# Kernel optimization log

Measured on AMD Instinct MI355X. Metric: run time of the kernel, lower is better.

Reference implementation:

```python
import jax, jax.numpy as jnp
import numpy as np

N = 100000
E = 1600000
D = 128
BN_EPS = 1e-5


def setup_inputs() -> dict:
    key = jax.random.key(0)
    ks = jax.random.split(key, 12)
    s = 1.0 / np.sqrt(D)
    x = jax.random.normal(ks[0], (N, D), dtype=jnp.float32)
    edge_index = jax.random.randint(ks[1], (2, E), 0, N, dtype=jnp.int64)
    # Linear weights stored as [in, out] (i.e. torch W.T)
    w1a = jax.random.uniform(ks[2], (D, D), jnp.float32, -s, s)
    b1a = jax.random.uniform(ks[3], (D,), jnp.float32, -s, s)
    w1b = jax.random.uniform(ks[4], (D, D), jnp.float32, -s, s)
    b1b = jax.random.uniform(ks[5], (D,), jnp.float32, -s, s)
    gamma2 = jnp.ones((D,), jnp.float32)
    beta2 = jnp.zeros((D,), jnp.float32)
    w2a = jax.random.uniform(ks[6], (D, D), jnp.float32, -s, s)
    b2a = jax.random.uniform(ks[7], (D,), jnp.float32, -s, s)
    w2b = jax.random.uniform(ks[8], (D, D), jnp.float32, -s, s)
    b2b = jax.random.uniform(ks[9], (D,), jnp.float32, -s, s)
    return dict(x=x, edge_index=edge_index, w1a=w1a, b1a=b1a, w1b=w1b, b1b=b1b,
                gamma2=gamma2, beta2=beta2, w2a=w2a, b2a=b2a, w2b=w2b, b2b=b2b)


def _gin_conv(h, src, dst, wa, ba, wb, bb):
    # GINConv (eps=0): nn(sum_{j in N(i)} h_j + h_i), then 2-layer MLP
    agg = jax.ops.segment_sum(h[src], dst, num_segments=h.shape[0])
    z = agg + h
    z = jax.nn.relu(z @ wa + ba)
    return z @ wb + bb


def reference(x, edge_index, w1a, b1a, w1b, b1b, gamma2, beta2, w2a, b2a, w2b, b2b):
    src, dst = edge_index[0], edge_index[1]
    h = _gin_conv(x, src, dst, w1a, b1a, w1b, b1b)
    h = jax.nn.relu(h)
    # BatchNorm1d in training mode: batch mean / biased variance
    mean = jnp.mean(h, axis=0)
    var = jnp.mean((h - mean) ** 2, axis=0)
    h = (h - mean) * jax.lax.rsqrt(var + BN_EPS) * gamma2 + beta2
    return _gin_conv(h, src, dst, w2a, b2a, w2b, b2b)
```

## Files before the change

kernel.cpp:

```cpp
#include <hip/hip_runtime.h>

#define NNODES 100000
#define NEDGES 1600000
#define DIM 128
#define BN_EPS 1e-5f
#define NBUCK 1024
#define NB_USED ((NNODES + 127) / 128)

typedef unsigned int uint;
typedef unsigned short ushort_t;
using bhalf8  = __attribute__((ext_vector_type(8))) short;
using u16x8   = __attribute__((ext_vector_type(8))) unsigned short;
using f32x4_t = __attribute__((ext_vector_type(4))) float;

__device__ __forceinline__ float bf2f(uint u16) {
    return __uint_as_float(u16 << 16);
}
__device__ __forceinline__ uint pack2_bf16rn(float a, float b) {
    uint ua = __float_as_uint(a); ua += 0x7FFFu + ((ua >> 16) & 1u);
    uint ub = __float_as_uint(b); ub += 0x7FFFu + ((ub >> 16) & 1u);
    return __builtin_amdgcn_perm(ub, ua, 0x07060302u);
}

__device__ __forceinline__ int edge_src(const int* ei, int fl, int e) {
    return fl ? ei[2 * e] : ei[e];
}
__device__ __forceinline__ int edge_dst(const int* ei, int fl, int e) {
    return fl ? ei[2 * (NEDGES + e)] : ei[NEDGES + e];
}

__global__ __launch_bounds__(256) void k_prep(const float* __restrict__ X,
                                              const int* __restrict__ ei,
                                              const float* __restrict__ w0,
                                              const float* __restrict__ w1,
                                              const float* __restrict__ w2,
                                              const float* __restrict__ w3,
                                              float* __restrict__ stats,
                                              int* __restrict__ flag,
                                              int* __restrict__ bcnt,
                                              ushort_t* __restrict__ wbuf,
                                              ushort_t* __restrict__ Xb) {
    int bid = blockIdx.x;
    int t = threadIdx.x;
    if (bid < 4) {
        const float* w = (bid == 0) ? w0 : (bid == 1) ? w1 : (bid == 2) ? w2 : w3;
        ushort_t* oh = wbuf + (size_t)bid * 16384;
        for (int i = t; i < 16384; i += 256) {
            int k = i >> 7, n = i & 127;
            uint u = __float_as_uint(w[i]);
            u += 0x7FFFu + ((u >> 16) & 1u);
            oh[n * 128 + k] = (ushort_t)(u >> 16);
        }
    } else if (bid == 4) {
        stats[t] = 0.0f;
        ((int4*)bcnt)[t] = make_int4(0, 0, 0, 0);
        if (t == 0) {
            int orr = 0;
            for (int i = 1; i < 128; i += 2) orr |= ei[i];
            *flag = (orr == 0) ? 1 : 0;
        }
    } else {
        size_t i = ((size_t)(bid - 5) * 256 + t) * 8;
        float4 a = *(const float4*)(X + i);
        float4 b = *(const float4*)(X + i + 4);
        union { uint4 q; u16x8 v; } o;
        o.q.x = pack2_bf16rn(a.x, a.y);
        o.q.y = pack2_bf16rn(a.z, a.w);
        o.q.z = pack2_bf16rn(b.x, b.y);
        o.q.w = pack2_bf16rn(b.z, b.w);
        *(u16x8*)(Xb + i) = o.v;
    }
}

__global__ __launch_bounds__(256) void k_bcount(const int* __restrict__ ei,
                                                const int* __restrict__ flag,
                                                int* __restrict__ bcnt) {
    __shared__ int h[NBUCK];
    int t = threadIdx.x;
    for (int i = t; i < NBUCK; i += 256) h[i] = 0;
    __syncthreads();
    int fl = *flag;
    int per = (NEDGES + gridDim.x - 1) / gridDim.x;
    int e0 = blockIdx.x * per;
    int e1 = min(e0 + per, NEDGES);
    for (int e = e0 + t; e < e1; e += 256)
        atomicAdd(&h[edge_dst(ei, fl, e) >> 7], 1);
    __syncthreads();
    for (int i = t; i < NBUCK; i += 256)
        if (h[i]) atomicAdd(&bcnt[i], h[i]);
}

__global__ __launch_bounds__(256) void k_bscan(const int* __restrict__ bcnt,
                                               int* __restrict__ bstart,
                                               int* __restrict__ bcur) {
    __shared__ int wtot[4];
    int t = threadIdx.x, lane = t & 63, w = t >> 6;
    int4 v = ((const int4*)bcnt)[t];
    int s = v.x + v.y + v.z + v.w;
    int sc = s;
#pragma unroll
    for (int d = 1; d < 64; d <<= 1) {
        int n = __shfl_up(sc, d, 64);
        if (lane >= d) sc += n;
    }
    if (lane == 63) wtot[w] = sc;
    __syncthreads();
    int woff = 0;
    for (int i = 0; i < w; ++i) woff += wtot[i];
    int excl = woff + sc - s;
    int o0 = excl, o1 = o0 + v.x, o2 = o1 + v.y, o3 = o2 + v.z;
    bstart[t * 4]     = o0;  bcur[t * 4]     = o0;
    bstart[t * 4 + 1] = o1;  bcur[t * 4 + 1] = o1;
    bstart[t * 4 + 2] = o2;  bcur[t * 4 + 2] = o2;
    bstart[t * 4 + 3] = o3;  bcur[t * 4 + 3] = o3;
    if (t == 255) bstart[NBUCK] = o3 + v.w;
}

__global__ __launch_bounds__(256) void k_bpair(const int* __restrict__ ei,
                                               const int* __restrict__ flag,
                                               int* __restrict__ bcur,
                                               int* __restrict__ pairs) {
    __shared__ int h[NBUCK];
    __shared__ int base[NBUCK];
    int t = threadIdx.x;
    for (int i = t; i < NBUCK; i += 256) h[i] = 0;
    __syncthreads();
    int fl = *flag;
    int per = (NEDGES + gridDim.x - 1) / gridDim.x;
    int e0 = blockIdx.x * per;
    int e1 = min(e0 + per, NEDGES);
    for (int e = e0 + t; e < e1; e += 256)
        atomicAdd(&h[edge_dst(ei, fl, e) >> 7], 1);
    __syncthreads();
    for (int i = t; i < NBUCK; i += 256) {
        int c = h[i];
        base[i] = c ? atomicAdd(&bcur[i], c) : 0;
    }
    __syncthreads();
    for (int i = t; i < NBUCK; i += 256) h[i] = 0;
    __syncthreads();
    for (int e = e0 + t; e < e1; e += 256) {
        int s = edge_src(ei, fl, e);
        int d = edge_dst(ei, fl, e);
        int b = d >> 7;
        int pos = atomicAdd(&h[b], 1);
        pairs[base[b] + pos] = (s << 7) | (d & 127);
    }
}

__global__ __launch_bounds__(256) void k_bsort(const int* __restrict__ pairs,
                                               const int* __restrict__ bstart,
                                               int* __restrict__ C,
                                               int* __restrict__ ssrc) {
    __shared__ int cnt[2048];
    __shared__ int off[2048];
    __shared__ int wtot[4];
    int b = blockIdx.x;
    int t = threadIdx.x, lane = t & 63, w = t >> 6;
    int s = bstart[b], e = bstart[b + 1];
    for (int i = t; i < 2048; i += 256) cnt[i] = 0;
    __syncthreads();
    for (int i = s + t; i < e; i += 256) {
        int p = pairs[i];
        atomicAdd(&cnt[(p & 127) * 16 + (p >> 20)], 1);
    }
    __syncthreads();
    int base = t * 8, loc[8], sum = 0;
#pragma unroll
    for (int j = 0; j < 8; ++j) { loc[j] = cnt[base + j]; sum += loc[j]; }
    int sc = sum;
#pragma unroll
    for (int d = 1; d < 64; d <<= 1) {
        int n = __shfl_up(sc, d, 64);
        if (lane >= d) sc += n;
    }
    if (lane == 63) wtot[w] = sc;
    __syncthreads();
    int woff = 0;
    for (int i = 0; i < w; ++i) woff += wtot[i];
    int run = woff + sc - sum;
#pragma unroll
    for (int j = 0; j < 8; ++j) { off[base + j] = run; run += loc[j]; }
    __syncthreads();
    if (t < 128) {
        int row = b * 128 + t;
        if (row < NNODES) C[row] = s + off[t * 16 + 15] + cnt[t * 16 + 15];
    }
    __syncthreads();
    for (int i = s + t; i < e; i += 256) {
        int p = pairs[i];
        int k = (p & 127) * 16 + (p >> 20);
        int pos = atomicAdd(&off[k], 1);
        ssrc[s + pos] = p >> 7;
    }
}

__device__ __forceinline__ void split8(const float4& f0, const float4& f1,
                                       bhalf8& h, bhalf8& l) {
    uint u[8] = { __float_as_uint(f0.x), __float_as_uint(f0.y),
                  __float_as_uint(f0.z), __float_as_uint(f0.w),
                  __float_as_uint(f1.x), __float_as_uint(f1.y),
                  __float_as_uint(f1.z), __float_as_uint(f1.w) };
    float fv[8] = { f0.x, f0.y, f0.z, f0.w, f1.x, f1.y, f1.z, f1.w };
    uint lu[8];
#pragma unroll
    for (int i = 0; i < 8; ++i) {
        float hf = __uint_as_float(u[i] & 0xffff0000u);
        lu[i] = __float_as_uint(fv[i] - hf);
    }
    union { uint4 q; bhalf8 s; } H, L;
    H.q.x = __builtin_amdgcn_perm(u[1], u[0], 0x07060302u);
    H.q.y = __builtin_amdgcn_perm(u[3], u[2], 0x07060302u);
    H.q.z = __builtin_amdgcn_perm(u[5], u[4], 0x07060302u);
    H.q.w = __builtin_amdgcn_perm(u[7], u[6], 0x07060302u);
    L.q.x = __builtin_amdgcn_perm(lu[1], lu[0], 0x07060302u);
    L.q.y = __builtin_amdgcn_perm(lu[3], lu[2], 0x07060302u);
    L.q.z = __builtin_amdgcn_perm(lu[5], lu[4], 0x07060302u);
    L.q.w = __builtin_amdgcn_perm(lu[7], lu[6], 0x07060302u);
    h = H.s; l = L.s;
}

template <bool BN, bool SELF_F32>
__global__ __launch_bounds__(256) void k_agg(const ushort_t* __restrict__ Xb,
                                             const float* __restrict__ Xf,
                                             float* __restrict__ Z,
                                             const int* __restrict__ ends,
                                             const int* __restrict__ ssrc,
                                             const float* __restrict__ stats,
                                             const float* __restrict__ gamma,
                                             const float* __restrict__ beta) {
    __shared__ float scs[128], shs[128];
    int t = threadIdx.x;
    if (BN) {
        if (t < 128) {
            float s  = stats[t];
            float sq = stats[128 + t];
            float mean = s / (float)NNODES;
            float var  = sq / (float)NNODES - mean * mean;
            float sc = gamma[t] * rsqrtf(var + BN_EPS);
            scs[t] = sc;
            shs[t] = beta[t] - mean * sc;
        }
        __syncthreads();
    }
    int g = t >> 4;
    int l = t & 15;
    int row = blockIdx.x * 16 + g;
    int c8 = l * 8;
    int start = (row == 0) ? 0 : ends[row - 1];
    int end = ends[row];

    float acc[8];
    if (SELF_F32) {
        float4 a0 = *(const float4*)(Xf + (size_t)row * DIM + c8);
        float4 a1 = *(const float4*)(Xf + (size_t)row * DIM + c8 + 4);
        acc[0] = a0.x; acc[1] = a0.y; acc[2] = a0.z; acc[3] = a0.w;
        acc[4] = a1.x; acc[5] = a1.y; acc[6] = a1.z; acc[7] = a1.w;
    } else {
        union { u16x8 v; uint u[4]; } sv;
        sv.v = *(const u16x8*)(Xb + (size_t)row * DIM + c8);
#pragma unroll
        for (int i = 0; i < 4; ++i) {
            acc[2 * i]     = bf2f(sv.u[i] & 0xffffu);
            acc[2 * i + 1] = __uint_as_float(sv.u[i] & 0xffff0000u);
        }
    }

    int e = start;
    for (; e + 7 < end; e += 8) {
        union { u16x8 v; uint u[4]; } nv[8];
#pragma unroll
        for (int i = 0; i < 8; ++i) {
            int s0 = ssrc[e + i];
            nv[i].v = *(const u16x8*)(Xb + (size_t)s0 * DIM + c8);
        }
#pragma unroll
        for (int i = 0; i < 8; ++i) {
#pragma unroll
            for (int j = 0; j < 4; ++j) {
                acc[2 * j]     += bf2f(nv[i].u[j] & 0xffffu);
                acc[2 * j + 1] += __uint_as_float(nv[i].u[j] & 0xffff0000u);
            }
        }
    }
    for (; e < end; ++e) {
        int s0 = ssrc[e];
        union { u16x8 v; uint u[4]; } nv;
        nv.v = *(const u16x8*)(Xb + (size_t)s0 * DIM + c8);
#pragma unroll
        for (int j = 0; j < 4; ++j) {
            acc[2 * j]     += bf2f(nv.u[j] & 0xffffu);
            acc[2 * j + 1] += __uint_as_float(nv.u[j] & 0xffff0000u);
        }
    }

    if (BN) {
        float4 sc0 = *(const float4*)(scs + c8);
        float4 sc1 = *(const float4*)(scs + c8 + 4);
        float4 sh0 = *(const float4*)(shs + c8);
        float4 sh1 = *(const float4*)(shs + c8 + 4);
        float cnt = (float)(end - start + 1);
        acc[0] = fmaf(acc[0], sc0.x, cnt * sh0.x);
        acc[1] = fmaf(acc[1], sc0.y, cnt * sh0.y);
        acc[2] = fmaf(acc[2], sc0.z, cnt * sh0.z);
        acc[3] = fmaf(acc[3], sc0.w, cnt * sh0.w);
        acc[4] = fmaf(acc[4], sc1.x, cnt * sh1.x);
        acc[5] = fmaf(acc[5], sc1.y, cnt * sh1.y);
        acc[6] = fmaf(acc[6], sc1.z, cnt * sh1.z);
        acc[7] = fmaf(acc[7], sc1.w, cnt * sh1.w);
    }
    float* zp = Z + (size_t)row * DIM + c8;
    *(float4*)zp       = make_float4(acc[0], acc[1], acc[2], acc[3]);
    *(float4*)(zp + 4) = make_float4(acc[4], acc[5], acc[6], acc[7]);
}

template <bool CONV1>
__global__ __launch_bounds__(256, 2) void k_mlp(const float* __restrict__ Z,
                                                const ushort_t* __restrict__ WAh,
                                                const ushort_t* __restrict__ WBh,
                                                const float* __restrict__ Ba,
                                                const float* __restrict__ Bb,
                                                float* __restrict__ OutF,
                                                ushort_t* __restrict__ OutB,
                                                float* __restrict__ stats) {
    __shared__ ushort_t wsl[16384];
    __shared__ float hbuf[64 * 128];
    __shared__ float lsum[128], lsq[128];
    char* hb = (char*)hbuf;

    int t = threadIdx.x;
    int w = t >> 6, l = t & 63;
    int lr = l & 15;
    int lg = l >> 4;
    int slane = (lr & 7) << 4;
    if (CONV1 && t < 128) { lsum[t] = 0.f; lsq[t] = 0.f; }

    int rowBase = blockIdx.x * 64 + w * 16;
    bool active = rowBase < NNODES;

#pragma unroll
    for (int i = 0; i < 8; ++i) {
        int c = i * 256 + t;
        uint4 v = ((const uint4*)WAh)[c];
        ((uint4*)wsl)[c ^ ((c >> 4) & 7)] = v;
    }
    int zrow = active ? (rowBase + lr) : 0;
    const float* zp = Z + (size_t)zrow * 128 + lg * 8;
    float4 zf[8];
#pragma unroll
    for (int ks = 0; ks < 4; ++ks) {
        zf[2 * ks]     = *(const float4*)(zp + ks * 32);
        zf[2 * ks + 1] = *(const float4*)(zp + ks * 32 + 4);
    }
    f32x4_t acc[8];
#pragma unroll
    for (int nt = 0; nt < 8; ++nt) {
        float b = Ba[nt * 16 + lr];
        acc[nt][0] = b; acc[nt][1] = b; acc[nt][2] = b; acc[nt][3] = b;
    }
    bhalf8 zh[4], zl[4];
#pragma unroll
    for (int ks = 0; ks < 4; ++ks) split8(zf[2 * ks], zf[2 * ks + 1], zh[ks], zl[ks]);
    __syncthreads();

#pragma unroll
    for (int ks = 0; ks < 4; ++ks) {
#pragma unroll
        for (int nt = 0; nt < 8; ++nt) {
            int waddr = ((nt * 16 + lr) << 8) + ((((ks << 6) + (lg << 4))) ^ slane);
            bhalf8 wh = *(const bhalf8*)((const char*)wsl + waddr);
            acc[nt] = __builtin_amdgcn_mfma_f32_16x16x32_bf16(zh[ks], wh, acc[nt], 0, 0, 0);
            acc[nt] = __builtin_amdgcn_mfma_f32_16x16x32_bf16(zl[ks], wh, acc[nt], 0, 0, 0);
        }
    }
#pragma unroll
    for (int nt = 0; nt < 8; ++nt) {
#pragma unroll
        for (int j = 0; j < 4; ++j) {
            int rl = w * 16 + lg * 4 + j;
            int boff = (rl * 512 + (nt * 16 + lr) * 4) ^ ((rl & 7) << 4);
            *(float*)(hb + boff) = fmaxf(acc[nt][j], 0.f);
        }
    }
    __syncthreads();

#pragma unroll
    for (int i = 0; i < 8; ++i) {
        int c = i * 256 + t;
        uint4 v = ((const uint4*)WBh)[c];
        ((uint4*)wsl)[c ^ ((c >> 4) & 7)] = v;
    }
    {
        int rl = w * 16 + lr;
        int swz = (rl & 7) << 4;
        int rbase = rl * 512 + lg * 32;
        float4 mf[8];
#pragma unroll
        for (int ks = 0; ks < 4; ++ks) {
            mf[2 * ks]     = *(const float4*)(hb + ((rbase + ks * 128) ^ swz));
            mf[2 * ks + 1] = *(const float4*)(hb + ((rbase + ks * 128 + 16) ^ swz));
        }
#pragma unroll
        for (int ks = 0; ks < 4; ++ks) split8(mf[2 * ks], mf[2 * ks + 1], zh[ks], zl[ks]);
    }
#pragma unroll
    for (int nt = 0; nt < 8; ++nt) {
        float b = Bb[nt * 16 + lr];
        acc[nt][0] = b; acc[nt][1] = b; acc[nt][2] = b; acc[nt][3] = b;
    }
    __syncthreads();

#pragma unroll
    for (int ks = 0; ks < 4; ++ks) {
#pragma unroll
        for (int nt = 0; nt < 8; ++nt) {
            int waddr = ((nt * 16 + lr) << 8) + ((((ks << 6) + (lg << 4))) ^ slane);
            bhalf8 wh = *(const bhalf8*)((const char*)wsl + waddr);
            acc[nt] = __builtin_amdgcn_mfma_f32_16x16x32_bf16(zh[ks], wh, acc[nt], 0, 0, 0);
            acc[nt] = __builtin_amdgcn_mfma_f32_16x16x32_bf16(zl[ks], wh, acc[nt], 0, 0, 0);
        }
    }

    if (CONV1 && active) {
#pragma unroll
        for (int nt = 0; nt < 8; ++nt) {
            float s = 0.f, q = 0.f;
#pragma unroll
            for (int j = 0; j < 4; ++j) {
                float v = fmaxf(acc[nt][j], 0.f);
                acc[nt][j] = v;
                s += v; q += v * v;
            }
            s += __shfl_xor(s, 16); s += __shfl_xor(s, 32);
            q += __shfl_xor(q, 16); q += __shfl_xor(q, 32);
            if (l < 16) {
                atomicAdd(&lsum[nt * 16 + l], s);
                atomicAdd(&lsq[nt * 16 + l], q);
            }
        }
    }
    __syncthreads();
#pragma unroll
    for (int nt = 0; nt < 8; ++nt) {
#pragma unroll
        for (int j = 0; j < 4; ++j) {
            int rl = w * 16 + lg * 4 + j;
            int boff = (rl * 512 + (nt * 16 + lr) * 4) ^ ((rl & 7) << 4);
            *(float*)(hb + boff) = acc[nt][j];
        }
    }
    if (CONV1) {
        __syncthreads();
        if (t < 128) {
            unsafeAtomicAdd(&stats[t], lsum[t]);
            unsafeAtomicAdd(&stats[128 + t], lsq[t]);
        }
    } else {
        __syncthreads();
    }
    {
        int r2 = t >> 2;
        int row = blockIdx.x * 64 + r2;
        if (row < NNODES) {
            int sw2 = (r2 & 7) << 4;
            int ch0 = (t & 3) * 8;
            if (CONV1) {
#pragma unroll
                for (int c = 0; c < 8; c += 2) {
                    float4 v0 = *(const float4*)(hb + ((r2 * 512 + (ch0 + c) * 16) ^ sw2));
                    float4 v1 = *(const float4*)(hb + ((r2 * 512 + (ch0 + c + 1) * 16) ^ sw2));
                    union { uint4 q; u16x8 v; } o;
                    o.q.x = pack2_bf16rn(v0.x, v0.y);
                    o.q.y = pack2_bf16rn(v0.z, v0.w);
                    o.q.z = pack2_bf16rn(v1.x, v1.y);
                    o.q.w = pack2_bf16rn(v1.z, v1.w);
                    *(u16x8*)(OutB + (size_t)row * 128 + (ch0 + c) * 4) = o.v;
                }
            } else {
#pragma unroll
                for (int c = 0; c < 8; ++c) {
                    float4 v = *(const float4*)(hb + ((r2 * 512 + (ch0 + c) * 16) ^ sw2));
                    *(float4*)(OutF + (size_t)row * 128 + (ch0 + c) * 4) = v;
                }
            }
        }
    }
}

extern "C" void kernel_launch(void* const* d_in, const int* in_sizes, int n_in,
                              void* d_out, int out_size, void* d_ws, size_t ws_size,
                              hipStream_t stream) {
    const float* x     = (const float*)d_in[0];
    const int*   ei    = (const int*)d_in[1];
    const float* w1a   = (const float*)d_in[2];
    const float* b1a   = (const float*)d_in[3];
    const float* w1b   = (const float*)d_in[4];
    const float* b1b   = (const float*)d_in[5];
    const float* gamma = (const float*)d_in[6];
    const float* beta  = (const float*)d_in[7];
    const float* w2a   = (const float*)d_in[8];
    const float* b2a   = (const float*)d_in[9];
    const float* w2b   = (const float*)d_in[10];
    const float* b2b   = (const float*)d_in[11];
    float* out = (float*)d_out;

    char*     ws     = (char*)d_ws;
    float*    stats  = (float*)ws;
    int*      flag   = (int*)(ws + 1024);
    int*      bcnt   = (int*)(ws + 4096);
    int*      bstart = (int*)(ws + 8192);
    int*      bcur   = (int*)(ws + 16384);
    int*      C      = (int*)(ws + 404096);
    int*      ssrc   = (int*)(ws + 804096);
    ushort_t* wbuf   = (ushort_t*)(ws + 0x700000);
    float*    zbuf   = (float*)(ws + 0x800000);
    int*      pairs  = (int*)(ws + 0x800000);

    ushort_t* xb  = (ushort_t*)d_out;
    ushort_t* hrb = (ushort_t*)d_out + (size_t)NNODES * DIM;

    const int aggBlocks  = NNODES / 16;
    const int prepBlocks = 5 + NNODES * DIM / (256 * 8);
    const int mlpBlocks  = (NNODES + 63) / 64;

    k_prep<<<prepBlocks, 256, 0, stream>>>(x, ei, w1a, w1b, w2a, w2b,
                                           stats, flag, bcnt, wbuf, xb);
    k_bcount<<<256, 256, 0, stream>>>(ei, flag, bcnt);
    k_bscan<<<1, 256, 0, stream>>>(bcnt, bstart, bcur);
    k_bpair<<<256, 256, 0, stream>>>(ei, flag, bcur, pairs);
    k_bsort<<<NB_USED, 256, 0, stream>>>(pairs, bstart, C, ssrc);
    k_agg<false, true><<<aggBlocks, 256, 0, stream>>>(xb, x, zbuf, C, ssrc,
                                                      nullptr, nullptr, nullptr);
    k_mlp<true><<<mlpBlocks, 256, 0, stream>>>(
        zbuf, wbuf, wbuf + 16384, b1a, b1b, nullptr, hrb, stats);
    k_agg<true, false><<<aggBlocks, 256, 0, stream>>>(hrb, nullptr, zbuf, C, ssrc,
                                                      stats, gamma, beta);
    k_mlp<false><<<mlpBlocks, 256, 0, stream>>>(
        zbuf, wbuf + 32768, wbuf + 49152, b2a, b2b, out, nullptr, nullptr);
}
```

Baseline: 306.1 us.

## Store aggregates in bf16, drop hi/lo split MFMAs, fuse histogram into prep

Result: no change. 305.4 us (-0.3%).

```diff
diff --git a/kernel.cpp b/kernel.cpp
--- a/kernel.cpp
+++ b/kernel.cpp
@@ -6,6 +6,7 @@
 #define BN_EPS 1e-5f
 #define NBUCK 1024
 #define NB_USED ((NNODES + 127) / 128)
+#define HISTB 64
 
 typedef unsigned int uint;
 typedef unsigned short ushort_t;
@@ -15,6 +16,11 @@
 
 __device__ __forceinline__ float bf2f(uint u16) {
     return __uint_as_float(u16 << 16);
+}
+__device__ __forceinline__ ushort_t f2bf(float f) {
+    uint u = __float_as_uint(f);
+    u += 0x7FFFu + ((u >> 16) & 1u);
+    return (ushort_t)(u >> 16);
 }
 __device__ __forceinline__ uint pack2_bf16rn(float a, float b) {
     uint ua = __float_as_uint(a); ua += 0x7FFFu + ((ua >> 16) & 1u);
@@ -37,9 +43,11 @@
                                               const float* __restrict__ w3,
                                               float* __restrict__ stats,
                                               int* __restrict__ flag,
-                                              int* __restrict__ bcnt,
+                                              int* __restrict__ parts,
                                               ushort_t* __restrict__ wbuf,
                                               ushort_t* __restrict__ Xb) {
+    __shared__ int h[NBUCK];
+    const int XB = NNODES * DIM / (256 * 8);
     int bid = blockIdx.x;
     int t = threadIdx.x;
     if (bid < 4) {
@@ -47,19 +55,16 @@
         ushort_t* oh = wbuf + (size_t)bid * 16384;
         for (int i = t; i < 16384; i += 256) {
             int k = i >> 7, n = i & 127;
-            uint u = __float_as_uint(w[i]);
-            u += 0x7FFFu + ((u >> 16) & 1u);
-            oh[n * 128 + k] = (ushort_t)(u >> 16);
+            oh[n * 128 + k] = f2bf(w[i]);
         }
     } else if (bid == 4) {
         stats[t] = 0.0f;
-        ((int4*)bcnt)[t] = make_int4(0, 0, 0, 0);
         if (t == 0) {
             int orr = 0;
             for (int i = 1; i < 128; i += 2) orr |= ei[i];
             *flag = (orr == 0) ? 1 : 0;
         }
-    } else {
+    } else if (bid < 5 + XB) {
         size_t i = ((size_t)(bid - 5) * 256 + t) * 8;
         float4 a = *(const float4*)(X + i);
         float4 b = *(const float4*)(X + i + 4);
@@ -69,33 +74,32 @@
         o.q.z = pack2_bf16rn(b.x, b.y);
         o.q.w = pack2_bf16rn(b.z, b.w);
         *(u16x8*)(Xb + i) = o.v;
-    }
-}
-
-__global__ __launch_bounds__(256) void k_bcount(const int* __restrict__ ei,
-                                                const int* __restrict__ flag,
-                                                int* __restrict__ bcnt) {
-    __shared__ int h[NBUCK];
-    int t = threadIdx.x;
-    for (int i = t; i < NBUCK; i += 256) h[i] = 0;
-    __syncthreads();
-    int fl = *flag;
-    int per = (NEDGES + gridDim.x - 1) / gridDim.x;
-    int e0 = blockIdx.x * per;
-    int e1 = min(e0 + per, NEDGES);
-    for (int e = e0 + t; e < e1; e += 256)
-        atomicAdd(&h[edge_dst(ei, fl, e) >> 7], 1);
-    __syncthreads();
-    for (int i = t; i < NBUCK; i += 256)
-        if (h[i]) atomicAdd(&bcnt[i], h[i]);
-}
-
-__global__ __launch_bounds__(256) void k_bscan(const int* __restrict__ bcnt,
+    } else {
+        int hb = bid - 5 - XB;
+        for (int i = t; i < NBUCK; i += 256) h[i] = 0;
+        __syncthreads();
+        int orr = 0;
+#pragma unroll
+        for (int i = 1; i < 64; i += 2) orr |= ei[i];
+        int fl = (orr == 0) ? 1 : 0;
+        int e0 = hb * (NEDGES / HISTB), e1 = e0 + NEDGES / HISTB;
+        for (int e = e0 + t; e < e1; e += 256)
+            atomicAdd(&h[edge_dst(ei, fl, e) >> 7], 1);
+        __syncthreads();
+        for (int i = t; i < NBUCK; i += 256) parts[hb * NBUCK + i] = h[i];
+    }
+}
+
+__global__ __launch_bounds__(256) void k_bscan(const int* __restrict__ parts,
                                                int* __restrict__ bstart,
                                                int* __restrict__ bcur) {
     __shared__ int wtot[4];
     int t = threadIdx.x, lane = t & 63, w = t >> 6;
-    int4 v = ((const int4*)bcnt)[t];
+    int4 v = make_int4(0, 0, 0, 0);
+    for (int b = 0; b < HISTB; ++b) {
+        int4 p = ((const int4*)(parts + b * NBUCK))[t];
+        v.x += p.x; v.y += p.y; v.z += p.z; v.w += p.w;
+    }
     int s = v.x + v.y + v.z + v.w;
     int sc = s;
 #pragma unroll
@@ -195,35 +199,10 @@
     }
 }
 
-__device__ __forceinline__ void split8(const float4& f0, const float4& f1,
-                                       bhalf8& h, bhalf8& l) {
-    uint u[8] = { __float_as_uint(f0.x), __float_as_uint(f0.y),
-                  __float_as_uint(f0.z), __float_as_uint(f0.w),
-                  __float_as_uint(f1.x), __float_as_uint(f1.y),
-                  __float_as_uint(f1.z), __float_as_uint(f1.w) };
-    float fv[8] = { f0.x, f0.y, f0.z, f0.w, f1.x, f1.y, f1.z, f1.w };
-    uint lu[8];
-#pragma unroll
-    for (int i = 0; i < 8; ++i) {
-        float hf = __uint_as_float(u[i] & 0xffff0000u);
-        lu[i] = __float_as_uint(fv[i] - hf);
-    }
-    union { uint4 q; bhalf8 s; } H, L;
-    H.q.x = __builtin_amdgcn_perm(u[1], u[0], 0x07060302u);
-    H.q.y = __builtin_amdgcn_perm(u[3], u[2], 0x07060302u);
-    H.q.z = __builtin_amdgcn_perm(u[5], u[4], 0x07060302u);
-    H.q.w = __builtin_amdgcn_perm(u[7], u[6], 0x07060302u);
-    L.q.x = __builtin_amdgcn_perm(lu[1], lu[0], 0x07060302u);
-    L.q.y = __builtin_amdgcn_perm(lu[3], lu[2], 0x07060302u);
-    L.q.z = __builtin_amdgcn_perm(lu[5], lu[4], 0x07060302u);
-    L.q.w = __builtin_amdgcn_perm(lu[7], lu[6], 0x07060302u);
-    h = H.s; l = L.s;
-}
-
 template <bool BN, bool SELF_F32>
 __global__ __launch_bounds__(256) void k_agg(const ushort_t* __restrict__ Xb,
                                              const float* __restrict__ Xf,
-                                             float* __restrict__ Z,
+                                             ushort_t* __restrict__ Zb,
                                              const int* __restrict__ ends,
                                              const int* __restrict__ ssrc,
                                              const float* __restrict__ stats,
@@ -309,24 +288,27 @@
         acc[6] = fmaf(acc[6], sc1.z, cnt * sh1.z);
         acc[7] = fmaf(acc[7], sc1.w, cnt * sh1.w);
     }
-    float* zp = Z + (size_t)row * DIM + c8;
-    *(float4*)zp       = make_float4(acc[0], acc[1], acc[2], acc[3]);
-    *(float4*)(zp + 4) = make_float4(acc[4], acc[5], acc[6], acc[7]);
+    union { uint4 q; u16x8 v; } o;
+    o.q.x = pack2_bf16rn(acc[0], acc[1]);
+    o.q.y = pack2_bf16rn(acc[2], acc[3]);
+    o.q.z = pack2_bf16rn(acc[4], acc[5]);
+    o.q.w = pack2_bf16rn(acc[6], acc[7]);
+    *(u16x8*)(Zb + (size_t)row * DIM + c8) = o.v;
 }
 
 template <bool CONV1>
-__global__ __launch_bounds__(256, 2) void k_mlp(const float* __restrict__ Z,
-                                                const ushort_t* __restrict__ WAh,
-                                                const ushort_t* __restrict__ WBh,
-                                                const float* __restrict__ Ba,
-                                                const float* __restrict__ Bb,
-                                                float* __restrict__ OutF,
-                                                ushort_t* __restrict__ OutB,
-                                                float* __restrict__ stats) {
+__global__ __launch_bounds__(256, CONV1 ? 3 : 2)
+void k_mlp(const ushort_t* __restrict__ Z,
+           const ushort_t* __restrict__ WAh,
+           const ushort_t* __restrict__ WBh,
+           const float* __restrict__ Ba,
+           const float* __restrict__ Bb,
+           float* __restrict__ OutF,
+           ushort_t* __restrict__ OutB,
+           float* __restrict__ stats) {
     __shared__ ushort_t wsl[16384];
-    __shared__ float hbuf[64 * 128];
+    __shared__ char hstage[CONV1 ? 16384 : 32768];
     __shared__ float lsum[128], lsq[128];
-    char* hb = (char*)hbuf;
 
     int t = threadIdx.x;
     int w = t >> 6, l = t & 63;
@@ -345,22 +327,16 @@
         ((uint4*)wsl)[c ^ ((c >> 4) & 7)] = v;
     }
     int zrow = active ? (rowBase + lr) : 0;
-    const float* zp = Z + (size_t)zrow * 128 + lg * 8;
-    float4 zf[8];
-#pragma unroll
-    for (int ks = 0; ks < 4; ++ks) {
-        zf[2 * ks]     = *(const float4*)(zp + ks * 32);
-        zf[2 * ks + 1] = *(const float4*)(zp + ks * 32 + 4);
-    }
+    const ushort_t* zp = Z + (size_t)zrow * 128 + lg * 8;
+    bhalf8 za[4];
+#pragma unroll
+    for (int ks = 0; ks < 4; ++ks) za[ks] = *(const bhalf8*)(zp + ks * 32);
     f32x4_t acc[8];
 #pragma unroll
     for (int nt = 0; nt < 8; ++nt) {
         float b = Ba[nt * 16 + lr];
         acc[nt][0] = b; acc[nt][1] = b; acc[nt][2] = b; acc[nt][3] = b;
     }
-    bhalf8 zh[4], zl[4];
-#pragma unroll
-    for (int ks = 0; ks < 4; ++ks) split8(zf[2 * ks], zf[2 * ks + 1], zh[ks], zl[ks]);
     __syncthreads();
 
 #pragma unroll
@@ -369,8 +345,7 @@
         for (int nt = 0; nt < 8; ++nt) {
             int waddr = ((nt * 16 + lr) << 8) + ((((ks << 6) + (lg << 4))) ^ slane);
             bhalf8 wh = *(const bhalf8*)((const char*)wsl + waddr);
-            acc[nt] = __builtin_amdgcn_mfma_f32_16x16x32_bf16(zh[ks], wh, acc[nt], 0, 0, 0);
-            acc[nt] = __builtin_amdgcn_mfma_f32_16x16x32_bf16(zl[ks], wh, acc[nt], 0, 0, 0);
+            acc[nt] = __builtin_amdgcn_mfma_f32_16x16x32_bf16(za[ks], wh, acc[nt], 0, 0, 0);
         }
     }
 #pragma unroll
@@ -378,8 +353,8 @@
 #pragma unroll
         for (int j = 0; j < 4; ++j) {
             int rl = w * 16 + lg * 4 + j;
-            int boff = (rl * 512 + (nt * 16 + lr) * 4) ^ ((rl & 7) << 4);
-            *(float*)(hb + boff) = fmaxf(acc[nt][j], 0.f);
+            int boff = (rl * 256 + (nt * 16 + lr) * 2) ^ ((rl & 7) << 4);
+            *(ushort_t*)(hstage + boff) = f2bf(fmaxf(acc[nt][j], 0.f));
         }
     }
     __syncthreads();
@@ -393,15 +368,9 @@
     {
         int rl = w * 16 + lr;
         int swz = (rl & 7) << 4;
-        int rbase = rl * 512 + lg * 32;
-        float4 mf[8];
-#pragma unroll
-        for (int ks = 0; ks < 4; ++ks) {
-            mf[2 * ks]     = *(const float4*)(hb + ((rbase + ks * 128) ^ swz));
-            mf[2 * ks + 1] = *(const float4*)(hb + ((rbase + ks * 128 + 16) ^ swz));
-        }
-#pragma unroll
-        for (int ks = 0; ks < 4; ++ks) split8(mf[2 * ks], mf[2 * ks + 1], zh[ks], zl[ks]);
+#pragma unroll
+        for (int ks = 0; ks < 4; ++ks)
+            za[ks] = *(const bhalf8*)(hstage + ((rl * 256 + (ks * 64 + lg * 16)) ^ swz));
     }
 #pragma unroll
     for (int nt = 0; nt < 8; ++nt) {
@@ -416,8 +385,7 @@
         for (int nt = 0; nt < 8; ++nt) {
             int waddr = ((nt * 16 + lr) << 8) + ((((ks << 6) + (lg << 4))) ^ slane);
             bhalf8 wh = *(const bhalf8*)((const char*)wsl + waddr);
-            acc[nt] = __builtin_amdgcn_mfma_f32_16x16x32_bf16(zh[ks], wh, acc[nt], 0, 0, 0);
-            acc[nt] = __builtin_amdgcn_mfma_f32_16x16x32_bf16(zl[ks], wh, acc[nt], 0, 0, 0);
+            acc[nt] = __builtin_amdgcn_mfma_f32_16x16x32_bf16(za[ks], wh, acc[nt], 0, 0, 0);
         }
     }
 
@@ -440,48 +408,52 @@
         }
     }
     __syncthreads();
-#pragma unroll
-    for (int nt = 0; nt < 8; ++nt) {
-#pragma unroll
-        for (int j = 0; j < 4; ++j) {
-            int rl = w * 16 + lg * 4 + j;
-            int boff = (rl * 512 + (nt * 16 + lr) * 4) ^ ((rl & 7) << 4);
-            *(float*)(hb + boff) = acc[nt][j];
-        }
-    }
     if (CONV1) {
+#pragma unroll
+        for (int nt = 0; nt < 8; ++nt) {
+#pragma unroll
+            for (int j = 0; j < 4; ++j) {
+                int rl = w * 16 + lg * 4 + j;
+                int boff = (rl * 256 + (nt * 16 + lr) * 2) ^ ((rl & 7) << 4);
+                *(ushort_t*)(hstage + boff) = f2bf(acc[nt][j]);
+            }
+        }
         __syncthreads();
         if (t < 128) {
             unsafeAtomicAdd(&stats[t], lsum[t]);
             unsafeAtomicAdd(&stats[128 + t], lsq[t]);
         }
+        int r2 = t >> 2;
+        int row = blockIdx.x * 64 + r2;
+        if (row < NNODES) {
+            int sw2 = (r2 & 7) << 4;
+#pragma unroll
+            for (int u = 0; u < 4; ++u) {
+                int uu = (t & 3) * 4 + u;
+                uint4 v = *(const uint4*)(hstage + ((r2 * 256 + uu * 16) ^ sw2));
+                *(uint4*)(OutB + (size_t)row * 128 + uu * 8) = v;
+            }
+        }
     } else {
+#pragma unroll
+        for (int nt = 0; nt < 8; ++nt) {
+#pragma unroll
+            for (int j = 0; j < 4; ++j) {
+                int rl = w * 16 + lg * 4 + j;
+                int boff = (rl * 512 + (nt * 16 + lr) * 4) ^ ((rl & 7) << 4);
+                *(float*)(hstage + boff) = acc[nt][j];
+            }
+        }
         __syncthreads();
-    }
-    {
         int r2 = t >> 2;
         int row = blockIdx.x * 64 + r2;
         if (row < NNODES) {
             int sw2 = (r2 & 7) << 4;
             int ch0 = (t & 3) * 8;
-            if (CONV1) {
-#pragma unroll
-                for (int c = 0; c < 8; c += 2) {
-                    float4 v0 = *(const float4*)(hb + ((r2 * 512 + (ch0 + c) * 16) ^ sw2));
-                    float4 v1 = *(const float4*)(hb + ((r2 * 512 + (ch0 + c + 1) * 16) ^ sw2));
-                    union { uint4 q; u16x8 v; } o;
-                    o.q.x = pack2_bf16rn(v0.x, v0.y);
-                    o.q.y = pack2_bf16rn(v0.z, v0.w);
-                    o.q.z = pack2_bf16rn(v1.x, v1.y);
-                    o.q.w = pack2_bf16rn(v1.z, v1.w);
-                    *(u16x8*)(OutB + (size_t)row * 128 + (ch0 + c) * 4) = o.v;
-                }
-            } else {
-#pragma unroll
-                for (int c = 0; c < 8; ++c) {
-                    float4 v = *(const float4*)(hb + ((r2 * 512 + (ch0 + c) * 16) ^ sw2));
-                    *(float4*)(OutF + (size_t)row * 128 + (ch0 + c) * 4) = v;
-                }
+#pragma unroll
+            for (int c = 0; c < 8; ++c) {
+                float4 v = *(const float4*)(hstage + ((r2 * 512 + (ch0 + c) * 16) ^ sw2));
+                *(float4*)(OutF + (size_t)row * 128 + (ch0 + c) * 4) = v;
             }
         }
     }
@@ -507,26 +479,25 @@
     char*     ws     = (char*)d_ws;
     float*    stats  = (float*)ws;
     int*      flag   = (int*)(ws + 1024);
-    int*      bcnt   = (int*)(ws + 4096);
     int*      bstart = (int*)(ws + 8192);
     int*      bcur   = (int*)(ws + 16384);
+    int*      parts  = (int*)(ws + 0x20000);
     int*      C      = (int*)(ws + 404096);
     int*      ssrc   = (int*)(ws + 804096);
     ushort_t* wbuf   = (ushort_t*)(ws + 0x700000);
-    float*    zbuf   = (float*)(ws + 0x800000);
+    ushort_t* zbuf   = (ushort_t*)(ws + 0x800000);
     int*      pairs  = (int*)(ws + 0x800000);
 
     ushort_t* xb  = (ushort_t*)d_out;
     ushort_t* hrb = (ushort_t*)d_out + (size_t)NNODES * DIM;
 
     const int aggBlocks  = NNODES / 16;
-    const int prepBlocks = 5 + NNODES * DIM / (256 * 8);
+    const int prepBlocks = 5 + NNODES * DIM / (256 * 8) + HISTB;
     const int mlpBlocks  = (NNODES + 63) / 64;
 
     k_prep<<<prepBlocks, 256, 0, stream>>>(x, ei, w1a, w1b, w2a, w2b,
-                                           stats, flag, bcnt, wbuf, xb);
-    k_bcount<<<256, 256, 0, stream>>>(ei, flag, bcnt);
-    k_bscan<<<1, 256, 0, stream>>>(bcnt, bstart, bcur);
+                                           stats, flag, parts, wbuf, xb);
+    k_bscan<<<1, 256, 0, stream>>>(parts, bstart, bcur);
     k_bpair<<<256, 256, 0, stream>>>(ei, flag, bcur, pairs);
     k_bsort<<<NB_USED, 256, 0, stream>>>(pairs, bstart, C, ssrc);
     k_agg<false, true><<<aggBlocks, 256, 0, stream>>>(xb, x, zbuf, C, ssrc,
```
